# Optimization experiments

Measured on AMD Instinct MI355X. Metric: run time of the kernel, lower is better.

The kernel has to match this reference:

```python
import jax, jax.numpy as jnp
import numpy as np

N = 25000   # nodes
E = 400000  # edges
F_IN = 128  # in_features
F_E = 16    # edge_features
C = 32      # channel_width
F_OUT = 1   # out_features
SLOPE = 0.01  # torch LeakyReLU default negative_slope


def leaky_relu(x):
    return jnp.where(x >= 0, x, SLOPE * x)


def setup_inputs() -> dict:
    key = jax.random.key(0)
    ks = jax.random.split(key, 12)
    x = jax.random.normal(ks[0], (N, F_IN), dtype=jnp.float32)
    edge_index = jax.random.randint(ks[1], (2, E), 0, N, dtype=jnp.int64)
    edge_attr = jax.random.normal(ks[2], (E, F_E), dtype=jnp.float32)
    # parameters (scaled like kaiming-ish fan-in init)
    W_in = jax.random.normal(ks[3], (F_IN, C), dtype=jnp.float32) / np.sqrt(F_IN)
    b_in = jnp.zeros((C,), dtype=jnp.float32)
    W_edge = jax.random.normal(ks[4], (F_E, C * C), dtype=jnp.float32) / np.sqrt(F_E)
    b_edge = jnp.zeros((C * C,), dtype=jnp.float32)
    W_root = jax.random.normal(ks[5], (C, C), dtype=jnp.float32) / np.sqrt(C)
    b_conv = jnp.zeros((C,), dtype=jnp.float32)
    W_out = jax.random.normal(ks[6], (C, F_OUT), dtype=jnp.float32) / np.sqrt(C)
    b_out = jnp.zeros((F_OUT,), dtype=jnp.float32)
    return {
        "x": x, "edge_index": edge_index, "edge_attr": edge_attr,
        "W_in": W_in, "b_in": b_in, "W_edge": W_edge, "b_edge": b_edge,
        "W_root": W_root, "b_conv": b_conv, "W_out": W_out, "b_out": b_out,
    }


def reference(x, edge_index, edge_attr, W_in, b_in, W_edge, b_edge,
              W_root, b_conv, W_out, b_out):
    # input projection (dropout = identity in eval mode)
    h = leaky_relu(x @ W_in + b_in)                       # [N, C]

    # NNConv layer (gnn_depth = 1):
    # per-edge weight matrix from edge_nn: Linear + LeakyReLU
    We = leaky_relu(edge_attr @ W_edge + b_edge)          # [E, C*C]
    We = We.reshape(E, C, C)                              # [E, C, C]
    src, dst = edge_index[0], edge_index[1]               # PyG: j=source, i=target
    # gather source node features, per-edge matvec, scatter-add to targets
    msg = jnp.einsum('ec,eco->eo', h[src], We)            # [E, C]
    aggr = jax.ops.segment_sum(msg, dst, num_segments=N)  # [N, C]
    h = aggr + h @ W_root + b_conv                        # root weight + bias
    h = leaky_relu(h)

    return h @ W_out + b_out                              # [N, F_OUT]
```

## Files before the change

kernel.cpp:

```cpp
#include <hip/hip_runtime.h>

#define NN 25000
#define EE 400000
#define FIN 128
#define FE 16
#define CH 32
#define SLOPE 0.01f
#define PROJ_BLOCKS 391
#define AUX_BLOCKS 32
#define WROW 24
#define WTP_SHORTS (1024 * WROW + 8)

typedef __attribute__((ext_vector_type(8))) short bf16x8;
typedef __attribute__((ext_vector_type(4))) float f32x4;

__device__ __forceinline__ float lrelu(float v) { return fmaxf(v, SLOPE * v); }

__device__ __forceinline__ f32x4 lrelu4(f32x4 v) {
    f32x4 s = v * SLOPE;
    f32x4 r;
    r[0] = fmaxf(v[0], s[0]); r[1] = fmaxf(v[1], s[1]);
    r[2] = fmaxf(v[2], s[2]); r[3] = fmaxf(v[3], s[3]);
    return r;
}

__device__ __forceinline__ short f2bf(float f) {
    union { float f; unsigned u; } v; v.f = f;
    unsigned r = (v.u + 0x7fffu + ((v.u >> 16) & 1u)) >> 16;
    return (short)r;
}

__global__ void __launch_bounds__(256)
k_pre(const float* __restrict__ x, const float* __restrict__ W_in,
      const float* __restrict__ b_in, const float* __restrict__ W_edge,
      const float* __restrict__ b_edge,
      float* __restrict__ h, float* __restrict__ aggr, short* __restrict__ WtP) {
    __shared__ short Wt1[CH * 136];
    int tid = threadIdx.x;

    if (blockIdx.x >= PROJ_BLOCKS) {
        int ab = blockIdx.x - PROJ_BLOCKS;
        if (ab < 4) {
            int co = ab * 256 + tid;
            short row[WROW] __attribute__((aligned(16)));
#pragma unroll
            for (int k = 0; k < 16; k++) row[k] = f2bf(W_edge[k * 1024 + co]);
            row[16] = f2bf(b_edge[co]);
#pragma unroll
            for (int k = 17; k < WROW; k++) row[k] = 0;
            uint4* dstp = (uint4*)(WtP + co * WROW);
            dstp[0] = ((uint4*)row)[0]; dstp[1] = ((uint4*)row)[1]; dstp[2] = ((uint4*)row)[2];
            if (ab == 0 && tid < 8) WtP[1024 * WROW + tid] = 0;
        } else {
            int t = (ab - 4) * 256 + tid;
            float4 z = make_float4(0.f, 0.f, 0.f, 0.f);
            for (int i = t; i < NN * CH / 4; i += (AUX_BLOCKS - 4) * 256)
                ((float4*)aggr)[i] = z;
        }
        return;
    }

#pragma unroll
    for (int i = 0; i < 16; i++) {
        int id = tid + 256 * i;
        int k = id >> 5, c = id & 31;
        Wt1[c * 136 + k] = f2bf(W_in[id]);
    }
    __syncthreads();

    int wave = tid >> 6, lane = tid & 63;
    int n16 = lane & 15, quad = lane >> 4;
    int node0 = blockIdx.x * 64 + wave * 16;

    f32x4 D[2];
#pragma unroll
    for (int ch = 0; ch < 2; ch++) {
        float bb = b_in[ch * 16 + n16];
        D[ch] = (f32x4){bb, bb, bb, bb};
    }
    int arow = node0 + n16; if (arow >= NN) arow = NN - 1;
#pragma unroll
    for (int kb = 0; kb < 4; kb++) {
        const float4* xp = (const float4*)(x + (size_t)arow * FIN + kb * 32 + quad * 8);
        float4 xa = xp[0], xb = xp[1];
        bf16x8 A = (bf16x8){f2bf(xa.x), f2bf(xa.y), f2bf(xa.z), f2bf(xa.w),
                            f2bf(xb.x), f2bf(xb.y), f2bf(xb.z), f2bf(xb.w)};
#pragma unroll
        for (int ch = 0; ch < 2; ch++) {
            bf16x8 B = *(const bf16x8*)&Wt1[(ch * 16 + n16) * 136 + kb * 32 + quad * 8];
            D[ch] = __builtin_amdgcn_mfma_f32_16x16x32_bf16(A, B, D[ch], 0, 0, 0);
        }
    }
#pragma unroll
    for (int ch = 0; ch < 2; ch++)
#pragma unroll
        for (int r = 0; r < 4; r++) {
            int nn = node0 + quad * 4 + r;
            if (nn < NN) h[(size_t)nn * CH + ch * 16 + n16] = lrelu(D[ch][r]);
        }
}

__global__ void __launch_bounds__(256, 2)
k_edge(const short* __restrict__ WtP,
       const float* __restrict__ ea,
       const int* __restrict__ src,
       const int* __restrict__ dst,
       const float* __restrict__ h,
       float* __restrict__ aggr) {
    __shared__ short WtL[WTP_SHORTS];
    __shared__ float hsT[CH * 132];

    int tid = threadIdx.x;
    int e0 = blockIdx.x * 128;

#pragma unroll
    for (int j = 0; j < 13; j++) {
        int idx = tid + 256 * j;
        if (idx < WTP_SHORTS / 8) ((uint4*)WtL)[idx] = ((const uint4*)WtP)[idx];
    }
    {
        int e = tid >> 1, half = tid & 1;
        int s = src[e0 + e];
        const float4* hp = (const float4*)(h + (size_t)s * CH + half * 16);
        float vv[16] __attribute__((aligned(16)));
        *(float4*)&vv[0] = hp[0]; *(float4*)&vv[4] = hp[1];
        *(float4*)&vv[8] = hp[2]; *(float4*)&vv[12] = hp[3];
#pragma unroll
        for (int j = 0; j < 16; j++) hsT[(half * 16 + j) * 132 + e] = vv[j];
    }
    __syncthreads();

    int wave = tid >> 6, lane = tid & 63;
    int n16 = lane & 15, quad = lane >> 4;
    int t0 = wave * 32, t1 = t0 + 16;

    bf16x8 A0 = (bf16x8){0,0,0,0,0,0,0,0}, A1 = A0;
    if (quad < 2) {
        const float4* p0 = (const float4*)(ea + (size_t)(e0 + t0 + n16) * FE + quad * 8);
        float4 a = p0[0], b = p0[1];
        A0 = (bf16x8){f2bf(a.x), f2bf(a.y), f2bf(a.z), f2bf(a.w),
                      f2bf(b.x), f2bf(b.y), f2bf(b.z), f2bf(b.w)};
        const float4* p1 = (const float4*)(ea + (size_t)(e0 + t1 + n16) * FE + quad * 8);
        a = p1[0]; b = p1[1];
        A1 = (bf16x8){f2bf(a.x), f2bf(a.y), f2bf(a.z), f2bf(a.w),
                      f2bf(b.x), f2bf(b.y), f2bf(b.z), f2bf(b.w)};
    } else if (quad == 2) {
        A0[0] = (short)0x3F80; A1[0] = (short)0x3F80;
    }

    f32x4 m0[2], m1[2];
    m0[0] = (f32x4){0,0,0,0}; m0[1] = m0[0]; m1[0] = m0[0]; m1[1] = m0[0];
    const f32x4 Z = (f32x4){0,0,0,0};

    const short* Bbase = WtL + n16 * WROW + quad * 8;
    const float* h0b = hsT + t0 + quad * 4;
    const float* h1b = hsT + t1 + quad * 4;

#pragma unroll 1
    for (int c4 = 0; c4 < 8; c4++) {
#pragma unroll
        for (int cc = 0; cc < 4; cc++) {
            int c = c4 * 4 + cc;
            f32x4 hc0 = *(const f32x4*)(h0b + c * 132);
            f32x4 hc1 = *(const f32x4*)(h1b + c * 132);
#pragma unroll
            for (int oh = 0; oh < 2; oh++) {
                int cb = c * 2 + oh;
                bf16x8 B = *(const bf16x8*)(Bbase + cb * (16 * WROW));
                f32x4 D0 = __builtin_amdgcn_mfma_f32_16x16x32_bf16(A0, B, Z, 0, 0, 0);
                f32x4 D1 = __builtin_amdgcn_mfma_f32_16x16x32_bf16(A1, B, Z, 0, 0, 0);
                m0[oh] += hc0 * lrelu4(D0);
                m1[oh] += hc1 * lrelu4(D1);
            }
        }
    }

#pragma unroll
    for (int r = 0; r < 4; r++) {
        int ed0 = dst[e0 + t0 + quad * 4 + r];
        int ed1 = dst[e0 + t1 + quad * 4 + r];
#pragma unroll
        for (int oh = 0; oh < 2; oh++) {
            unsafeAtomicAdd(&aggr[(size_t)ed0 * CH + oh * 16 + n16], m0[oh][r]);
            unsafeAtomicAdd(&aggr[(size_t)ed1 * CH + oh * 16 + n16], m1[oh][r]);
        }
    }
}

__global__ void k_node(const float* __restrict__ aggr,
                       const float* __restrict__ h,
                       const float* __restrict__ W_root,
                       const float* __restrict__ b_conv,
                       const float* __restrict__ W_out,
                       const float* __restrict__ b_out,
                       float* __restrict__ out) {
    __shared__ float WrT[CH * CH];
    __shared__ float Wo[CH];
    __shared__ float bc[CH];
    int tid = threadIdx.x;
#pragma unroll
    for (int i = 0; i < 4; i++) {
        int t = tid + 256 * i;
        WrT[t] = W_root[(t & 31) * CH + (t >> 5)];
    }
    if (tid < CH) { Wo[tid] = W_out[tid]; bc[tid] = b_conv[tid]; }
    __syncthreads();
    int n = blockIdx.x * 256 + tid;
    if (n >= NN) return;
    float hr[CH], ag[CH];
#pragma unroll
    for (int i = 0; i < CH / 4; i++) {
        ((float4*)hr)[i] = ((const float4*)(h + (size_t)n * CH))[i];
        ((float4*)ag)[i] = ((const float4*)(aggr + (size_t)n * CH))[i];
    }
    float acc = b_out[0];
#pragma unroll 1
    for (int o = 0; o < CH; o++) {
        float t = ag[o] + bc[o];
        const f32x4* wr = (const f32x4*)&WrT[o * CH];
#pragma unroll
        for (int c4 = 0; c4 < 8; c4++) {
            f32x4 w = wr[c4];
            const float* hc = &hr[c4 * 4];
            t = fmaf(hc[0], w[0], t); t = fmaf(hc[1], w[1], t);
            t = fmaf(hc[2], w[2], t); t = fmaf(hc[3], w[3], t);
        }
        acc = fmaf(lrelu(t), Wo[o], acc);
    }
    out[n] = acc;
}

extern "C" void kernel_launch(void* const* d_in, const int* in_sizes, int n_in,
                              void* d_out, int out_size, void* d_ws, size_t ws_size,
                              hipStream_t stream) {
    const float* x      = (const float*)d_in[0];
    const int*   ei     = (const int*)d_in[1];
    const float* ea     = (const float*)d_in[2];
    const float* W_in   = (const float*)d_in[3];
    const float* b_in   = (const float*)d_in[4];
    const float* W_edge = (const float*)d_in[5];
    const float* b_edge = (const float*)d_in[6];
    const float* W_root = (const float*)d_in[7];
    const float* b_conv = (const float*)d_in[8];
    const float* W_out  = (const float*)d_in[9];
    const float* b_out  = (const float*)d_in[10];
    float* out  = (float*)d_out;
    float* h    = (float*)d_ws;
    float* aggr = h + (size_t)NN * CH;
    short* WtP  = (short*)(aggr + (size_t)NN * CH);

    k_pre<<<PROJ_BLOCKS + AUX_BLOCKS, 256, 0, stream>>>(x, W_in, b_in, W_edge, b_edge,
                                                        h, aggr, WtP);
    k_edge<<<EE / 128, 256, 0, stream>>>(WtP, ea, ei, ei + EE, h, aggr);
    k_node<<<(NN + 255) / 256, 256, 0, stream>>>(aggr, h, W_root, b_conv, W_out, b_out, out);
}
```

Measured before the change: 189.2 us.

## Rewrite node kernel with bf16 MFMA, fully unroll edge loop, vector max

```diff
diff --git a/kernel.cpp b/kernel.cpp
--- a/kernel.cpp
+++ b/kernel.cpp
@@ -18,10 +18,14 @@
 
 __device__ __forceinline__ f32x4 lrelu4(f32x4 v) {
     f32x4 s = v * SLOPE;
+#if __has_builtin(__builtin_elementwise_max)
+    return __builtin_elementwise_max(v, s);
+#else
     f32x4 r;
     r[0] = fmaxf(v[0], s[0]); r[1] = fmaxf(v[1], s[1]);
     r[2] = fmaxf(v[2], s[2]); r[3] = fmaxf(v[3], s[3]);
     return r;
+#endif
 }
 
 __device__ __forceinline__ short f2bf(float f) {
@@ -156,7 +160,7 @@
     const float* h0b = hsT + t0 + quad * 4;
     const float* h1b = hsT + t1 + quad * 4;
 
-#pragma unroll 1
+#pragma unroll
     for (int c4 = 0; c4 < 8; c4++) {
 #pragma unroll
         for (int cc = 0; cc < 4; cc++) {
@@ -187,47 +191,68 @@
     }
 }
 
-__global__ void k_node(const float* __restrict__ aggr,
-                       const float* __restrict__ h,
-                       const float* __restrict__ W_root,
-                       const float* __restrict__ b_conv,
-                       const float* __restrict__ W_out,
-                       const float* __restrict__ b_out,
-                       float* __restrict__ out) {
-    __shared__ float WrT[CH * CH];
-    __shared__ float Wo[CH];
-    __shared__ float bc[CH];
+__global__ void __launch_bounds__(256)
+k_node(const float* __restrict__ aggr,
+       const float* __restrict__ h,
+       const float* __restrict__ W_root,
+       const float* __restrict__ b_conv,
+       const float* __restrict__ W_out,
+       const float* __restrict__ b_out,
+       float* __restrict__ out) {
+    __shared__ short WrB[CH * 40];
+    __shared__ float WoS[CH];
     int tid = threadIdx.x;
-#pragma unroll
-    for (int i = 0; i < 4; i++) {
-        int t = tid + 256 * i;
-        WrT[t] = W_root[(t & 31) * CH + (t >> 5)];
-    }
-    if (tid < CH) { Wo[tid] = W_out[tid]; bc[tid] = b_conv[tid]; }
+    if (tid < 128) {
+        int o = tid >> 2, c0 = (tid & 3) * 8;
+        short tmp[8] __attribute__((aligned(16)));
+#pragma unroll
+        for (int j = 0; j < 8; j++) tmp[j] = f2bf(W_root[(c0 + j) * CH + o]);
+        *(bf16x8*)&WrB[o * 40 + c0] = *(bf16x8*)tmp;
+    } else if (tid < 160) {
+        WoS[tid - 128] = W_out[tid - 128];
+    }
     __syncthreads();
-    int n = blockIdx.x * 256 + tid;
-    if (n >= NN) return;
-    float hr[CH], ag[CH];
-#pragma unroll
-    for (int i = 0; i < CH / 4; i++) {
-        ((float4*)hr)[i] = ((const float4*)(h + (size_t)n * CH))[i];
-        ((float4*)ag)[i] = ((const float4*)(aggr + (size_t)n * CH))[i];
-    }
-    float acc = b_out[0];
-#pragma unroll 1
-    for (int o = 0; o < CH; o++) {
-        float t = ag[o] + bc[o];
-        const f32x4* wr = (const f32x4*)&WrT[o * CH];
-#pragma unroll
-        for (int c4 = 0; c4 < 8; c4++) {
-            f32x4 w = wr[c4];
-            const float* hc = &hr[c4 * 4];
-            t = fmaf(hc[0], w[0], t); t = fmaf(hc[1], w[1], t);
-            t = fmaf(hc[2], w[2], t); t = fmaf(hc[3], w[3], t);
-        }
-        acc = fmaf(lrelu(t), Wo[o], acc);
-    }
-    out[n] = acc;
+
+    int wave = tid >> 6, lane = tid & 63;
+    int n16 = lane & 15, quad = lane >> 4;
+    int node0 = blockIdx.x * 64 + wave * 16;
+
+    int arow = node0 + n16; if (arow >= NN) arow = NN - 1;
+    const float4* hp = (const float4*)(h + (size_t)arow * CH + quad * 8);
+    float4 ha = hp[0], hb = hp[1];
+    bf16x8 A = (bf16x8){f2bf(ha.x), f2bf(ha.y), f2bf(ha.z), f2bf(ha.w),
+                        f2bf(hb.x), f2bf(hb.y), f2bf(hb.z), f2bf(hb.w)};
+    float bc0 = b_conv[n16], bc1 = b_conv[16 + n16];
+    f32x4 C0, C1;
+#pragma unroll
+    for (int r = 0; r < 4; r++) {
+        int nr = node0 + quad * 4 + r; int cr = (nr < NN) ? nr : NN - 1;
+        C0[r] = aggr[(size_t)cr * CH + n16] + bc0;
+        C1[r] = aggr[(size_t)cr * CH + 16 + n16] + bc1;
+    }
+    bf16x8 B0 = *(const bf16x8*)&WrB[n16 * 40 + quad * 8];
+    bf16x8 B1 = *(const bf16x8*)&WrB[(16 + n16) * 40 + quad * 8];
+    f32x4 D0 = __builtin_amdgcn_mfma_f32_16x16x32_bf16(A, B0, C0, 0, 0, 0);
+    f32x4 D1 = __builtin_amdgcn_mfma_f32_16x16x32_bf16(A, B1, C1, 0, 0, 0);
+
+    float w0 = WoS[n16], w1 = WoS[16 + n16];
+    f32x4 p;
+#pragma unroll
+    for (int r = 0; r < 4; r++)
+        p[r] = lrelu(D0[r]) * w0 + lrelu(D1[r]) * w1;
+#pragma unroll
+    for (int mk = 1; mk < 16; mk <<= 1) {
+#pragma unroll
+        for (int r = 0; r < 4; r++) p[r] += __shfl_xor(p[r], mk, 64);
+    }
+    if (n16 == 0) {
+        float bo = b_out[0];
+#pragma unroll
+        for (int r = 0; r < 4; r++) {
+            int nr = node0 + quad * 4 + r;
+            if (nr < NN) out[nr] = p[r] + bo;
+        }
+    }
 }
 
 extern "C" void kernel_launch(void* const* d_in, const int* in_sizes, int n_in,
@@ -252,5 +277,5 @@
     k_pre<<<PROJ_BLOCKS + AUX_BLOCKS, 256, 0, stream>>>(x, W_in, b_in, W_edge, b_edge,
                                                         h, aggr, WtP);
     k_edge<<<EE / 128, 256, 0, stream>>>(WtP, ea, ei, ei + EE, h, aggr);
-    k_node<<<(NN + 255) / 256, 256, 0, stream>>>(aggr, h, W_root, b_conv, W_out, b_out, out);
-}
+    k_node<<<PROJ_BLOCKS, 256, 0, stream>>>(aggr, h, W_root, b_conv, W_out, b_out, out);
+}
```

After: 167.2 us. -11.6%, faster.
